# Optimization experiments

Hardware: AMD Instinct MI355X
Metric: run time of the kernel (lower is better)

Reference implementation:

```python
import jax, jax.numpy as jnp
import numpy as np

EMBED_DIM = 1024
HEADS = 16
D_HEAD = EMBED_DIM // HEADS
B, S = 2, 2048


def setup_inputs() -> dict:
    key = jax.random.key(0)
    ks = jax.random.split(key, 7)
    scale = 1.0 / np.sqrt(EMBED_DIM)
    inp = {
        "key": jax.random.normal(ks[0], (B, S, EMBED_DIM), dtype=jnp.float32),
        "query": jax.random.normal(ks[1], (B, S, EMBED_DIM), dtype=jnp.float32),
        "value": jax.random.normal(ks[2], (B, S, EMBED_DIM), dtype=jnp.float32),
        # causal mask, broadcastable to [B, H, Sq, Sk]
        "mask": jnp.tril(jnp.ones((S, S), dtype=bool))[None, None, :, :],
        # torch nn.Linear weights: [out_features, in_features], applied as x @ W.T
        "Wq": jax.random.normal(ks[3], (EMBED_DIM, EMBED_DIM), dtype=jnp.float32) * scale,
        "Wk": jax.random.normal(ks[4], (EMBED_DIM, EMBED_DIM), dtype=jnp.float32) * scale,
        "Wv": jax.random.normal(ks[5], (EMBED_DIM, EMBED_DIM), dtype=jnp.float32) * scale,
        "Wo": jax.random.normal(ks[6], (EMBED_DIM, EMBED_DIM), dtype=jnp.float32) * scale,
    }
    return inp


def reference(key, query, value, mask, Wq, Wk, Wv, Wo):
    b, sq, _ = query.shape
    sk = key.shape[1]
    # projections (torch Linear: x @ W.T), reshape to [B, H, S, Dh]
    q = (query @ Wq.T).reshape(b, sq, HEADS, D_HEAD).transpose(0, 2, 1, 3)
    k = (key @ Wk.T).reshape(b, sk, HEADS, D_HEAD).transpose(0, 2, 1, 3)
    v = (value @ Wv.T).reshape(b, sk, HEADS, D_HEAD).transpose(0, 2, 1, 3)
    # scaled dot-product scores [B, H, Sq, Sk]
    scores = jnp.einsum("bhqd,bhkd->bhqk", q, k) / jnp.sqrt(jnp.float32(D_HEAD))
    scores = jnp.where(mask, scores, jnp.float32(-1e9))
    attn = jax.nn.softmax(scores, axis=-1)
    # dropout p=0.0 -> identity
    out = jnp.einsum("bhqk,bhkd->bhqd", attn, v)  # [B, H, Sq, Dh]
    out = out.transpose(0, 2, 1, 3).reshape(b, sq, EMBED_DIM)
    return out @ Wo.T
```

## Files before the change

kernel.cpp:

```cpp
#include <hip/hip_runtime.h>
#include <stdint.h>


typedef unsigned short ushort_t;
typedef __attribute__((ext_vector_type(8))) __bf16 bf16x8;
typedef __attribute__((ext_vector_type(4))) float floatx4;

#define EMBED 1024
#define SEQ   2048
#define NH    16
#define DH    64
#define QK_SCALE 0.18033688011112042f

__device__ inline ushort_t f2b(float x) {
  unsigned u = __float_as_uint(x);
  u += 0x7FFFu + ((u >> 16) & 1u);
  return (ushort_t)(u >> 16);
}

__device__ inline unsigned pk2(float a, float b) {
  unsigned ua = __float_as_uint(a) + 0x8000u;
  unsigned ub = __float_as_uint(b) + 0x8000u;
  return __builtin_amdgcn_perm(ub, ua, 0x07060302u);
}

__device__ inline void gl_lds16(const ushort_t* g, ushort_t* l) {
  __builtin_amdgcn_global_load_lds(
      (const __attribute__((address_space(1))) unsigned int*)g,
      (__attribute__((address_space(3))) unsigned int*)l, 16, 0, 0);
}

struct CvtArgs {
  const float* src[16];
  ushort_t*    dst[16];
  float        scale[16];
};

__global__ __launch_bounds__(256) void cvt_kernel(CvtArgs a) {
  const int chunk = blockIdx.x >> 9;
  const int off = ((blockIdx.x & 511) << 11) + (threadIdx.x << 3);
  const float sc = a.scale[chunk];
  const float4* s = (const float4*)(a.src[chunk] + off);
  float4 f0 = s[0], f1 = s[1];
  union { ushort_t u[8]; uint4 v; } o;
  o.u[0] = f2b(f0.x * sc); o.u[1] = f2b(f0.y * sc);
  o.u[2] = f2b(f0.z * sc); o.u[3] = f2b(f0.w * sc);
  o.u[4] = f2b(f1.x * sc); o.u[5] = f2b(f1.y * sc);
  o.u[6] = f2b(f1.z * sc); o.u[7] = f2b(f1.w * sc);
  *(uint4*)(a.dst[chunk] + off) = o.v;
}

__device__ inline void store_sub(char* __restrict__ Cv, const int mode,
                                 const int ldc, const int row, const int col,
                                 const floatx4& acc) {
  if (mode == 0) {
    ushort_t* C = (ushort_t*)Cv;
#pragma unroll
    for (int r = 0; r < 4; ++r)
      C[(size_t)(row + r) * ldc + col] = f2b(acc[r]);
  } else if (mode == 1) {
    float* C = (float*)Cv;
#pragma unroll
    for (int r = 0; r < 4; ++r)
      C[(size_t)(row + r) * ldc + col] = acc[r];
  } else {
    ushort_t* C = (ushort_t*)Cv;
    const int b = row >> 11, s = row & 2047;
    const int h = col >> 6, d = col & 63;
    uint2 pk;
    pk.x = pk2(acc[0], acc[1]);
    pk.y = pk2(acc[2], acc[3]);
    *(uint2*)&C[(size_t)((b * NH + h) * DH + d) * SEQ + s] = pk;
  }
}

__device__ inline void gemm512_core(const ushort_t* __restrict__ A,
                                    const ushort_t* __restrict__ W,
                                    char* __restrict__ Cv, const int mode,
                                    const int ldc, const int m0, const int n0) {
  __shared__ ushort_t As[32 * 512];
  __shared__ ushort_t Bs[16 * 512];
  const int tid  = threadIdx.x;
  const int lane = tid & 63;
  const int wid  = tid >> 6;
  const int lm   = lane & 15;
  const int quad = lane >> 4;
  const int wm   = wid >> 1;
  const int wn   = wid & 1;

  floatx4 zero = {0.f, 0.f, 0.f, 0.f};
  floatx4 acc[4][4];
#pragma unroll
  for (int i = 0; i < 4; ++i)
#pragma unroll
    for (int j = 0; j < 4; ++j) acc[i][j] = zero;

  for (int k0 = 0; k0 < EMBED; k0 += 64) {
    __syncthreads();
#pragma unroll
    for (int u = 0; u < 6; ++u) {
      const int c   = wid * 6 + u;
      const int cb  = c & 31;
      const int sub = cb >> 1;
      const int kc  = (cb & 1) * 32 + quad * 8;
      if (c < 32)
        gl_lds16(A + (size_t)(m0 + sub * 16 + lm) * EMBED + k0 + kc, &As[cb * 512]);
      else
        gl_lds16(W + (size_t)(n0 + sub * 16 + lm) * EMBED + k0 + kc, &Bs[cb * 512]);
    }
    __syncthreads();

#pragma unroll
    for (int ks = 0; ks < 2; ++ks) {
      bf16x8 a[4], b[4];
#pragma unroll
      for (int i = 0; i < 4; ++i)
        a[i] = *(const bf16x8*)&As[((wm * 4 + i) * 2 + ks) * 512 + lane * 8];
#pragma unroll
      for (int j = 0; j < 4; ++j)
        b[j] = *(const bf16x8*)&Bs[((wn * 4 + j) * 2 + ks) * 512 + lane * 8];
#pragma unroll
      for (int i = 0; i < 4; ++i)
#pragma unroll
        for (int j = 0; j < 4; ++j)
          acc[i][j] = __builtin_amdgcn_mfma_f32_16x16x32_bf16(a[i], b[j], acc[i][j], 0, 0, 0);
    }
  }

#pragma unroll
  for (int i = 0; i < 4; ++i) {
    const int row = m0 + wm * 64 + i * 16 + quad * 4;
#pragma unroll
    for (int j = 0; j < 4; ++j)
      store_sub(Cv, mode, ldc, row, n0 + wn * 64 + j * 16 + lm, acc[i][j]);
  }
}

struct QkvArgs {
  const ushort_t* A[3];
  const ushort_t* W[3];
  char*           C[3];
};

__global__ __launch_bounds__(512, 4) void qkv_gemm(QkvArgs q) {
  const int z = blockIdx.z;
  gemm512_core(q.A[z], q.W[z], q.C[z], z == 2 ? 2 : 0, EMBED,
               blockIdx.x * 256, blockIdx.y * 128);
}

__global__ __launch_bounds__(256, 4) void o_gemm(const ushort_t* __restrict__ A,
                                                 const ushort_t* __restrict__ W,
                                                 float* __restrict__ C) {
  __shared__ ushort_t As[16 * 512];
  __shared__ ushort_t Bs[8 * 512];
  const int m0 = blockIdx.x * 128, n0 = blockIdx.y * 64;
  const int tid  = threadIdx.x;
  const int lane = tid & 63;
  const int wid  = tid >> 6;
  const int lm   = lane & 15;
  const int quad = lane >> 4;
  const int wm   = wid >> 1;
  const int wn   = wid & 1;

  floatx4 zero = {0.f, 0.f, 0.f, 0.f};
  floatx4 acc[4][2];
#pragma unroll
  for (int i = 0; i < 4; ++i)
#pragma unroll
    for (int j = 0; j < 2; ++j) acc[i][j] = zero;

  for (int k0 = 0; k0 < EMBED; k0 += 64) {
    __syncthreads();
#pragma unroll
    for (int u = 0; u < 6; ++u) {
      const int c   = wid * 6 + u;
      const int cb  = (c < 16) ? c : (c - 16);
      const int sub = cb >> 1;
      const int kc  = (cb & 1) * 32 + quad * 8;
      if (c < 16)
        gl_lds16(A + (size_t)(m0 + sub * 16 + lm) * EMBED + k0 + kc, &As[cb * 512]);
      else
        gl_lds16(W + (size_t)(n0 + sub * 16 + lm) * EMBED + k0 + kc, &Bs[cb * 512]);
    }
    __syncthreads();

#pragma unroll
    for (int ks = 0; ks < 2; ++ks) {
      bf16x8 a[4], b[2];
#pragma unroll
      for (int i = 0; i < 4; ++i)
        a[i] = *(const bf16x8*)&As[((wm * 4 + i) * 2 + ks) * 512 + lane * 8];
#pragma unroll
      for (int j = 0; j < 2; ++j)
        b[j] = *(const bf16x8*)&Bs[((wn * 2 + j) * 2 + ks) * 512 + lane * 8];
#pragma unroll
      for (int i = 0; i < 4; ++i)
#pragma unroll
        for (int j = 0; j < 2; ++j)
          acc[i][j] = __builtin_amdgcn_mfma_f32_16x16x32_bf16(a[i], b[j], acc[i][j], 0, 0, 0);
    }
  }

#pragma unroll
  for (int i = 0; i < 4; ++i) {
    const int row = m0 + wm * 64 + i * 16 + quad * 4;
#pragma unroll
    for (int j = 0; j < 2; ++j) {
      const int col = n0 + wn * 32 + j * 16 + lm;
#pragma unroll
      for (int r = 0; r < 4; ++r)
        C[(size_t)(row + r) * EMBED + col] = acc[i][j][r];
    }
  }
}

__global__ __launch_bounds__(256, 4) void attn_kernel(const ushort_t* __restrict__ Qp,
                                                      const ushort_t* __restrict__ Kp,
                                                      const ushort_t* __restrict__ VpT,
                                                      ushort_t* __restrict__ Ob) {
  __shared__ ushort_t Qs[8 * 512];
  __shared__ ushort_t Ks[2][8 * 512];
  __shared__ ushort_t VTs[2][8 * 512];
  const int L = blockIdx.x;
  const int s8 = (L >> 5) & 7;
  const int g  = L >> 8;
  const int qb = (g == 0) ? s8
               : (g == 1) ? (15 - s8)
               : (g == 2) ? (16 + s8)
                          : (31 - s8);
  const int bh = L & 31;
  const int h = bh & (NH - 1), b = bh >> 4;
  const int tid = threadIdx.x, lane = tid & 63, wid = tid >> 6;
  const int lm = lane & 15, quad = lane >> 4;
  const size_t qkbase = ((size_t)b * SEQ) * EMBED + h * DH;
  const size_t vtbase = ((size_t)(b * NH + h)) * DH * SEQ;

#pragma unroll
  for (int u = 0; u < 2; ++u) {
    const int c = wid * 2 + u;
    gl_lds16(Qp + qkbase + (size_t)(qb * 64 + (c >> 1) * 16 + lm) * EMBED
                 + (c & 1) * 32 + quad * 8,
             &Qs[c * 512]);
  }
#pragma unroll
  for (int u = 0; u < 4; ++u) {
    const int t = wid * 4 + u;
    const int cb = t & 7, sub = cb >> 1, half = cb & 1;
    if (t < 8)
      gl_lds16(Kp + qkbase + (size_t)(sub * 16 + lm) * EMBED + half * 32 + quad * 8,
               &Ks[0][cb * 512]);
    else
      gl_lds16(VpT + vtbase + (size_t)(sub * 16 + lm) * SEQ + half * 32 + quad * 8,
               &VTs[0][cb * 512]);
  }
  asm volatile("s_waitcnt vmcnt(4)" ::: "memory");
  bf16x8 qf[2];
#pragma unroll
  for (int ks = 0; ks < 2; ++ks)
    qf[ks] = *(const bf16x8*)&Qs[(wid * 2 + ks) * 512 + lane * 8];
  ushort_t* pwb = &Qs[wid * 1024];

  float l_part = 0.f;
  floatx4 zero = {0.f, 0.f, 0.f, 0.f};
  floatx4 o_acc[4];
#pragma unroll
  for (int d = 0; d < 4; ++d) o_acc[d] = zero;

  for (int kt = 0; kt <= qb; ++kt) {
    const int cur = kt & 1;
    asm volatile("s_waitcnt vmcnt(0)" ::: "memory");
    __syncthreads();
    if (kt < qb) {
      const int kn = kt + 1;
#pragma unroll
      for (int u = 0; u < 4; ++u) {
        const int t = wid * 4 + u;
        const int cb = t & 7, sub = cb >> 1, half = cb & 1;
        if (t < 8)
          gl_lds16(Kp + qkbase + (size_t)(kn * 64 + sub * 16 + lm) * EMBED
                       + half * 32 + quad * 8,
                   &Ks[cur ^ 1][cb * 512]);
        else
          gl_lds16(VpT + vtbase + (size_t)(sub * 16 + lm) * SEQ
                       + kn * 64 + half * 32 + quad * 8,
                   &VTs[cur ^ 1][cb * 512]);
      }
    }

    floatx4 s_acc[4];
#pragma unroll
    for (int i = 0; i < 4; ++i) s_acc[i] = zero;
#pragma unroll
    for (int ks = 0; ks < 2; ++ks)
#pragma unroll
      for (int i = 0; i < 4; ++i) {
        bf16x8 kf = *(const bf16x8*)&Ks[cur][(i * 2 + ks) * 512 + lane * 8];
        s_acc[i] = __builtin_amdgcn_mfma_f32_16x16x32_bf16(kf, qf[ks], s_acc[i], 0, 0, 0);
      }

    const bool diag = (kt == qb);
#pragma unroll
    for (int i = 0; i < 4; ++i) {
      const int sH = i >> 1;
      const int quadB = ((i & 1) << 1) | (quad >> 1);
      const int gkk = kt * 64 + i * 16 + quad * 4;
      float p[4];
#pragma unroll
      for (int r = 0; r < 4; ++r) p[r] = __builtin_amdgcn_exp2f(s_acc[i][r]);
      if (diag) {
        const int gq = qb * 64 + wid * 16 + lm;
#pragma unroll
        for (int r = 0; r < 4; ++r)
          if (gkk + r > gq) p[r] = 0.f;
      }
#pragma unroll
      for (int r = 0; r < 4; ++r) l_part += p[r];
      uint2 pk;
      pk.x = pk2(p[0], p[1]);
      pk.y = pk2(p[2], p[3]);
      *(uint2*)&pwb[sH * 512 + (quadB * 16 + lm) * 8 + ((quad & 1) << 2)] = pk;
    }
    asm volatile("s_waitcnt lgkmcnt(0)" ::: "memory");

#pragma unroll
    for (int sH = 0; sH < 2; ++sH) {
      bf16x8 pf = *(const bf16x8*)&pwb[sH * 512 + lane * 8];
#pragma unroll
      for (int d = 0; d < 4; ++d) {
        bf16x8 vf = *(const bf16x8*)&VTs[cur][(d * 2 + sH) * 512 + lane * 8];
        o_acc[d] = __builtin_amdgcn_mfma_f32_16x16x32_bf16(vf, pf, o_acc[d], 0, 0, 0);
      }
    }
  }

  {
    float l = l_part;
    l += __shfl_xor(l, 16, 64);
    l += __shfl_xor(l, 32, 64);
    const float inv_l = 1.0f / l;
    const size_t orow = qkbase + (size_t)(qb * 64 + wid * 16 + lm) * EMBED;
#pragma unroll
    for (int d = 0; d < 4; ++d) {
      uint2 pk;
      pk.x = pk2(o_acc[d][0] * inv_l, o_acc[d][1] * inv_l);
      pk.y = pk2(o_acc[d][2] * inv_l, o_acc[d][3] * inv_l);
      *(uint2*)&Ob[orow + d * 16 + quad * 4] = pk;
    }
  }
}

extern "C" void kernel_launch(void* const* d_in, const int* in_sizes, int n_in,
                              void* d_out, int out_size, void* d_ws, size_t ws_size,
                              hipStream_t stream) {
  const float* key   = (const float*)d_in[0];
  const float* query = (const float*)d_in[1];
  const float* value = (const float*)d_in[2];
  const float* Wq = (const float*)d_in[4];
  const float* Wk = (const float*)d_in[5];
  const float* Wv = (const float*)d_in[6];
  const float* Wo = (const float*)d_in[7];

  char* ws = (char*)d_ws;
  const size_t MB = 1024 * 1024;
  ushort_t* Xk  = (ushort_t*)(ws + 0 * MB);
  ushort_t* Xq  = (ushort_t*)(ws + 8 * MB);
  ushort_t* Xv  = (ushort_t*)(ws + 16 * MB);
  ushort_t* Wqb = (ushort_t*)(ws + 24 * MB);
  ushort_t* Wkb = (ushort_t*)(ws + 26 * MB);
  ushort_t* Wvb = (ushort_t*)(ws + 28 * MB);
  ushort_t* Wob = (ushort_t*)(ws + 30 * MB);
  ushort_t* Qp  = (ushort_t*)(ws + 32 * MB);
  ushort_t* Kp  = (ushort_t*)(ws + 40 * MB);
  ushort_t* VpT = (ushort_t*)(ws + 48 * MB);
  ushort_t* Ob  = (ushort_t*)(ws + 56 * MB);

  CvtArgs ca;
  const size_t CE = 1048576;
  for (int c = 0; c < 16; ++c) ca.scale[c] = 1.0f;
  for (int c = 0; c < 4; ++c) { ca.src[c]     = key   + c * CE; ca.dst[c]     = Xk + c * CE; }
  for (int c = 0; c < 4; ++c) { ca.src[4 + c] = query + c * CE; ca.dst[4 + c] = Xq + c * CE; }
  for (int c = 0; c < 4; ++c) { ca.src[8 + c] = value + c * CE; ca.dst[8 + c] = Xv + c * CE; }
  ca.src[12] = Wq; ca.dst[12] = Wqb; ca.scale[12] = QK_SCALE;
  ca.src[13] = Wk; ca.dst[13] = Wkb;
  ca.src[14] = Wv; ca.dst[14] = Wvb;
  ca.src[15] = Wo; ca.dst[15] = Wob;
  cvt_kernel<<<8192, 256, 0, stream>>>(ca);

  QkvArgs qa;
  qa.A[0] = Xq; qa.W[0] = Wqb; qa.C[0] = (char*)Qp;
  qa.A[1] = Xk; qa.W[1] = Wkb; qa.C[1] = (char*)Kp;
  qa.A[2] = Xv; qa.W[2] = Wvb; qa.C[2] = (char*)VpT;
  qkv_gemm<<<dim3(16, 8, 3), 512, 0, stream>>>(qa);

  attn_kernel<<<1024, 256, 0, stream>>>(Qp, Kp, VpT, Ob);

  o_gemm<<<dim3(32, 16), 256, 0, stream>>>(Ob, Wob, (float*)d_out);
}
```

Baseline: 238.8 us.

## Fuse conversion with QKV GEMM and attention with output GEMM via grid barriers

Merges the four kernel launches into two persistent-style kernels. The first does the fp32-to-bf16 conversion and then the QKV projection behind a software grid barrier. The second runs attention, with some blocks handling two tiles, and then the output projection behind a second barrier. This removes launch gaps and tail idle time between stages. In exchange it relies on every block being co-resident, since the spin barrier deadlocks otherwise, and it adds a memset plus atomic spinning.

```diff
diff --git a/kernel.cpp b/kernel.cpp
--- a/kernel.cpp
+++ b/kernel.cpp
@@ -30,24 +30,17 @@
       (__attribute__((address_space(3))) unsigned int*)l, 16, 0, 0);
 }
 
-struct CvtArgs {
-  const float* src[16];
-  ushort_t*    dst[16];
-  float        scale[16];
-};
-
-__global__ __launch_bounds__(256) void cvt_kernel(CvtArgs a) {
-  const int chunk = blockIdx.x >> 9;
-  const int off = ((blockIdx.x & 511) << 11) + (threadIdx.x << 3);
-  const float sc = a.scale[chunk];
-  const float4* s = (const float4*)(a.src[chunk] + off);
-  float4 f0 = s[0], f1 = s[1];
-  union { ushort_t u[8]; uint4 v; } o;
-  o.u[0] = f2b(f0.x * sc); o.u[1] = f2b(f0.y * sc);
-  o.u[2] = f2b(f0.z * sc); o.u[3] = f2b(f0.w * sc);
-  o.u[4] = f2b(f1.x * sc); o.u[5] = f2b(f1.y * sc);
-  o.u[6] = f2b(f1.z * sc); o.u[7] = f2b(f1.w * sc);
-  *(uint4*)(a.dst[chunk] + off) = o.v;
+__device__ inline void grid_arrive_wait(unsigned* cnt, unsigned target) {
+  __syncthreads();
+  __threadfence();
+  if (threadIdx.x == 0) {
+    __hip_atomic_fetch_add(cnt, 1u, __ATOMIC_ACQ_REL, __HIP_MEMORY_SCOPE_AGENT);
+    while (__hip_atomic_load(cnt, __ATOMIC_ACQUIRE, __HIP_MEMORY_SCOPE_AGENT)
+           < target)
+      __builtin_amdgcn_s_sleep(2);
+  }
+  __syncthreads();
+  __threadfence();
 }
 
 __device__ inline void store_sub(char* __restrict__ Cv, const int mode,
@@ -136,92 +129,49 @@
   }
 }
 
-struct QkvArgs {
+struct FusedA {
+  const float*    src[16];
+  ushort_t*       dst[16];
+  float           scale[16];
   const ushort_t* A[3];
   const ushort_t* W[3];
   char*           C[3];
+  unsigned*       bar;
 };
 
-__global__ __launch_bounds__(512, 4) void qkv_gemm(QkvArgs q) {
-  const int z = blockIdx.z;
-  gemm512_core(q.A[z], q.W[z], q.C[z], z == 2 ? 2 : 0, EMBED,
-               blockIdx.x * 256, blockIdx.y * 128);
-}
-
-__global__ __launch_bounds__(256, 4) void o_gemm(const ushort_t* __restrict__ A,
-                                                 const ushort_t* __restrict__ W,
-                                                 float* __restrict__ C) {
-  __shared__ ushort_t As[16 * 512];
-  __shared__ ushort_t Bs[8 * 512];
-  const int m0 = blockIdx.x * 128, n0 = blockIdx.y * 64;
-  const int tid  = threadIdx.x;
-  const int lane = tid & 63;
-  const int wid  = tid >> 6;
-  const int lm   = lane & 15;
-  const int quad = lane >> 4;
-  const int wm   = wid >> 1;
-  const int wn   = wid & 1;
-
-  floatx4 zero = {0.f, 0.f, 0.f, 0.f};
-  floatx4 acc[4][2];
-#pragma unroll
-  for (int i = 0; i < 4; ++i)
-#pragma unroll
-    for (int j = 0; j < 2; ++j) acc[i][j] = zero;
-
-  for (int k0 = 0; k0 < EMBED; k0 += 64) {
-    __syncthreads();
-#pragma unroll
-    for (int u = 0; u < 6; ++u) {
-      const int c   = wid * 6 + u;
-      const int cb  = (c < 16) ? c : (c - 16);
-      const int sub = cb >> 1;
-      const int kc  = (cb & 1) * 32 + quad * 8;
-      if (c < 16)
-        gl_lds16(A + (size_t)(m0 + sub * 16 + lm) * EMBED + k0 + kc, &As[cb * 512]);
-      else
-        gl_lds16(W + (size_t)(n0 + sub * 16 + lm) * EMBED + k0 + kc, &Bs[cb * 512]);
-    }
-    __syncthreads();
-
-#pragma unroll
-    for (int ks = 0; ks < 2; ++ks) {
-      bf16x8 a[4], b[2];
-#pragma unroll
-      for (int i = 0; i < 4; ++i)
-        a[i] = *(const bf16x8*)&As[((wm * 4 + i) * 2 + ks) * 512 + lane * 8];
-#pragma unroll
-      for (int j = 0; j < 2; ++j)
-        b[j] = *(const bf16x8*)&Bs[((wn * 2 + j) * 2 + ks) * 512 + lane * 8];
-#pragma unroll
-      for (int i = 0; i < 4; ++i)
-#pragma unroll
-        for (int j = 0; j < 2; ++j)
-          acc[i][j] = __builtin_amdgcn_mfma_f32_16x16x32_bf16(a[i], b[j], acc[i][j], 0, 0, 0);
-    }
-  }
-
-#pragma unroll
-  for (int i = 0; i < 4; ++i) {
-    const int row = m0 + wm * 64 + i * 16 + quad * 4;
-#pragma unroll
-    for (int j = 0; j < 2; ++j) {
-      const int col = n0 + wn * 32 + j * 16 + lm;
-#pragma unroll
-      for (int r = 0; r < 4; ++r)
-        C[(size_t)(row + r) * EMBED + col] = acc[i][j][r];
-    }
-  }
-}
-
-__global__ __launch_bounds__(256, 4) void attn_kernel(const ushort_t* __restrict__ Qp,
-                                                      const ushort_t* __restrict__ Kp,
-                                                      const ushort_t* __restrict__ VpT,
-                                                      ushort_t* __restrict__ Ob) {
-  __shared__ ushort_t Qs[8 * 512];
-  __shared__ ushort_t Ks[2][8 * 512];
-  __shared__ ushort_t VTs[2][8 * 512];
-  const int L = blockIdx.x;
+__global__ __launch_bounds__(512, 4) void cvt_qkv_kernel(FusedA fa) {
+  {
+    const unsigned idx0 = blockIdx.x * 512u + threadIdx.x;
+#pragma unroll 1
+    for (int p = 0; p < 11; ++p) {
+      const unsigned idx = p * 196608u + idx0;
+      if (idx < 2097152u) {
+        const int chunk = idx >> 17;
+        const unsigned off = (idx & 131071u) << 3;
+        const float sc = fa.scale[chunk];
+        const float4* s = (const float4*)(fa.src[chunk] + off);
+        float4 f0 = s[0], f1 = s[1];
+        union { ushort_t u[8]; uint4 v; } o;
+        o.u[0] = f2b(f0.x * sc); o.u[1] = f2b(f0.y * sc);
+        o.u[2] = f2b(f0.z * sc); o.u[3] = f2b(f0.w * sc);
+        o.u[4] = f2b(f1.x * sc); o.u[5] = f2b(f1.y * sc);
+        o.u[6] = f2b(f1.z * sc); o.u[7] = f2b(f1.w * sc);
+        *(uint4*)(fa.dst[chunk] + off) = o.v;
+      }
+    }
+  }
+  grid_arrive_wait(fa.bar, 384u);
+  const int t = blockIdx.x;
+  const int z = t >> 7, y = (t >> 4) & 7, x = t & 15;
+  gemm512_core(fa.A[z], fa.W[z], fa.C[z], z == 2 ? 2 : 0, EMBED,
+               x * 256, y * 128);
+}
+
+__device__ void attn_body(const ushort_t* __restrict__ Qp,
+                          const ushort_t* __restrict__ Kp,
+                          const ushort_t* __restrict__ VpT,
+                          ushort_t* __restrict__ Ob,
+                          ushort_t* smem, const int L) {
   const int s8 = (L >> 5) & 7;
   const int g  = L >> 8;
   const int qb = (g == 0) ? s8
@@ -234,6 +184,7 @@
   const int lm = lane & 15, quad = lane >> 4;
   const size_t qkbase = ((size_t)b * SEQ) * EMBED + h * DH;
   const size_t vtbase = ((size_t)(b * NH + h)) * DH * SEQ;
+  ushort_t* Qs = smem;
 
 #pragma unroll
   for (int u = 0; u < 2; ++u) {
@@ -244,14 +195,14 @@
   }
 #pragma unroll
   for (int u = 0; u < 4; ++u) {
-    const int t = wid * 4 + u;
-    const int cb = t & 7, sub = cb >> 1, half = cb & 1;
-    if (t < 8)
+    const int tt = wid * 4 + u;
+    const int cb = tt & 7, sub = cb >> 1, half = cb & 1;
+    if (tt < 8)
       gl_lds16(Kp + qkbase + (size_t)(sub * 16 + lm) * EMBED + half * 32 + quad * 8,
-               &Ks[0][cb * 512]);
+               &smem[4096 + cb * 512]);
     else
       gl_lds16(VpT + vtbase + (size_t)(sub * 16 + lm) * SEQ + half * 32 + quad * 8,
-               &VTs[0][cb * 512]);
+               &smem[12288 + cb * 512]);
   }
   asm volatile("s_waitcnt vmcnt(4)" ::: "memory");
   bf16x8 qf[2];
@@ -268,22 +219,26 @@
 
   for (int kt = 0; kt <= qb; ++kt) {
     const int cur = kt & 1;
+    ushort_t* Kc = smem + 4096 + cur * 4096;
+    ushort_t* Vc = smem + 12288 + cur * 4096;
     asm volatile("s_waitcnt vmcnt(0)" ::: "memory");
     __syncthreads();
     if (kt < qb) {
       const int kn = kt + 1;
+      ushort_t* Knx = smem + 4096 + (cur ^ 1) * 4096;
+      ushort_t* Vnx = smem + 12288 + (cur ^ 1) * 4096;
 #pragma unroll
       for (int u = 0; u < 4; ++u) {
-        const int t = wid * 4 + u;
-        const int cb = t & 7, sub = cb >> 1, half = cb & 1;
-        if (t < 8)
+        const int tt = wid * 4 + u;
+        const int cb = tt & 7, sub = cb >> 1, half = cb & 1;
+        if (tt < 8)
           gl_lds16(Kp + qkbase + (size_t)(kn * 64 + sub * 16 + lm) * EMBED
                        + half * 32 + quad * 8,
-                   &Ks[cur ^ 1][cb * 512]);
+                   &Knx[cb * 512]);
         else
           gl_lds16(VpT + vtbase + (size_t)(sub * 16 + lm) * SEQ
                        + kn * 64 + half * 32 + quad * 8,
-                   &VTs[cur ^ 1][cb * 512]);
+                   &Vnx[cb * 512]);
       }
     }
 
@@ -294,7 +249,7 @@
     for (int ks = 0; ks < 2; ++ks)
 #pragma unroll
       for (int i = 0; i < 4; ++i) {
-        bf16x8 kf = *(const bf16x8*)&Ks[cur][(i * 2 + ks) * 512 + lane * 8];
+        bf16x8 kf = *(const bf16x8*)&Kc[(i * 2 + ks) * 512 + lane * 8];
         s_acc[i] = __builtin_amdgcn_mfma_f32_16x16x32_bf16(kf, qf[ks], s_acc[i], 0, 0, 0);
       }
 
@@ -327,7 +282,7 @@
       bf16x8 pf = *(const bf16x8*)&pwb[sH * 512 + lane * 8];
 #pragma unroll
       for (int d = 0; d < 4; ++d) {
-        bf16x8 vf = *(const bf16x8*)&VTs[cur][(d * 2 + sH) * 512 + lane * 8];
+        bf16x8 vf = *(const bf16x8*)&Vc[(d * 2 + sH) * 512 + lane * 8];
         o_acc[d] = __builtin_amdgcn_mfma_f32_16x16x32_bf16(vf, pf, o_acc[d], 0, 0, 0);
       }
     }
@@ -347,6 +302,98 @@
       *(uint2*)&Ob[orow + d * 16 + quad * 4] = pk;
     }
   }
+}
+
+__device__ void o_core(const ushort_t* __restrict__ A,
+                       const ushort_t* __restrict__ W,
+                       float* __restrict__ C, ushort_t* smem,
+                       const int bx, const int by) {
+  ushort_t* As = smem;
+  ushort_t* Bs = smem + 8192;
+  const int m0 = bx * 128, n0 = by * 64;
+  const int tid  = threadIdx.x;
+  const int lane = tid & 63;
+  const int wid  = tid >> 6;
+  const int lm   = lane & 15;
+  const int quad = lane >> 4;
+  const int wm   = wid >> 1;
+  const int wn   = wid & 1;
+
+  floatx4 zero = {0.f, 0.f, 0.f, 0.f};
+  floatx4 acc[4][2];
+#pragma unroll
+  for (int i = 0; i < 4; ++i)
+#pragma unroll
+    for (int j = 0; j < 2; ++j) acc[i][j] = zero;
+
+  for (int k0 = 0; k0 < EMBED; k0 += 64) {
+    __syncthreads();
+#pragma unroll
+    for (int u = 0; u < 6; ++u) {
+      const int c   = wid * 6 + u;
+      const int cb  = (c < 16) ? c : (c - 16);
+      const int sub = cb >> 1;
+      const int kc  = (cb & 1) * 32 + quad * 8;
+      if (c < 16)
+        gl_lds16(A + (size_t)(m0 + sub * 16 + lm) * EMBED + k0 + kc, &As[cb * 512]);
+      else
+        gl_lds16(W + (size_t)(n0 + sub * 16 + lm) * EMBED + k0 + kc, &Bs[cb * 512]);
+    }
+    __syncthreads();
+
+#pragma unroll
+    for (int ks = 0; ks < 2; ++ks) {
+      bf16x8 a[4], b[2];
+#pragma unroll
+      for (int i = 0; i < 4; ++i)
+        a[i] = *(const bf16x8*)&As[((wm * 4 + i) * 2 + ks) * 512 + lane * 8];
+#pragma unroll
+      for (int j = 0; j < 2; ++j)
+        b[j] = *(const bf16x8*)&Bs[((wn * 2 + j) * 2 + ks) * 512 + lane * 8];
+#pragma unroll
+      for (int i = 0; i < 4; ++i)
+#pragma unroll
+        for (int j = 0; j < 2; ++j)
+          acc[i][j] = __builtin_amdgcn_mfma_f32_16x16x32_bf16(a[i], b[j], acc[i][j], 0, 0, 0);
+    }
+  }
+
+#pragma unroll
+  for (int i = 0; i < 4; ++i) {
+    const int row = m0 + wm * 64 + i * 16 + quad * 4;
+#pragma unroll
+    for (int j = 0; j < 2; ++j) {
+      const int col = n0 + wn * 32 + j * 16 + lm;
+#pragma unroll
+      for (int r = 0; r < 4; ++r)
+        C[(size_t)(row + r) * EMBED + col] = acc[i][j][r];
+    }
+  }
+}
+
+struct FusedB {
+  const ushort_t* Qp;
+  const ushort_t* Kp;
+  const ushort_t* VpT;
+  ushort_t*       Ob;
+  const ushort_t* Wob;
+  float*          out;
+  unsigned*       bar;
+};
+
+__global__ __launch_bounds__(256, 4) void attn_o_kernel(FusedB fb) {
+  __shared__ ushort_t smem[20480];
+  const int r = blockIdx.x;
+  if (r < 256) {
+    attn_body(fb.Qp, fb.Kp, fb.VpT, fb.Ob, smem, r);
+    __syncthreads();
+    attn_body(fb.Qp, fb.Kp, fb.VpT, fb.Ob, smem, 256 + r);
+  } else {
+    attn_body(fb.Qp, fb.Kp, fb.VpT, fb.Ob, smem, 256 + r);
+  }
+  grid_arrive_wait(fb.bar, 768u);
+  if (r < 512)
+    o_core(fb.Ob, fb.Wob, fb.out, smem, r & 31, r >> 5);
 }
 
 extern "C" void kernel_launch(void* const* d_in, const int* in_sizes, int n_in,
@@ -373,26 +420,31 @@
   ushort_t* Kp  = (ushort_t*)(ws + 40 * MB);
   ushort_t* VpT = (ushort_t*)(ws + 48 * MB);
   ushort_t* Ob  = (ushort_t*)(ws + 56 * MB);
-
-  CvtArgs ca;
+  unsigned* bar = (unsigned*)(ws + 64 * MB);
+
+  hipMemsetAsync(bar, 0, 128, stream);
+
+  FusedA fa;
   const size_t CE = 1048576;
-  for (int c = 0; c < 16; ++c) ca.scale[c] = 1.0f;
-  for (int c = 0; c < 4; ++c) { ca.src[c]     = key   + c * CE; ca.dst[c]     = Xk + c * CE; }
-  for (int c = 0; c < 4; ++c) { ca.src[4 + c] = query + c * CE; ca.dst[4 + c] = Xq + c * CE; }
-  for (int c = 0; c < 4; ++c) { ca.src[8 + c] = value + c * CE; ca.dst[8 + c] = Xv + c * CE; }
-  ca.src[12] = Wq; ca.dst[12] = Wqb; ca.scale[12] = QK_SCALE;
-  ca.src[13] = Wk; ca.dst[13] = Wkb;
-  ca.src[14] = Wv; ca.dst[14] = Wvb;
-  ca.src[15] = Wo; ca.dst[15] = Wob;
-  cvt_kernel<<<8192, 256, 0, stream>>>(ca);
-
-  QkvArgs qa;
-  qa.A[0] = Xq; qa.W[0] = Wqb; qa.C[0] = (char*)Qp;
-  qa.A[1] = Xk; qa.W[1] = Wkb; qa.C[1] = (char*)Kp;
-  qa.A[2] = Xv; qa.W[2] = Wvb; qa.C[2] = (char*)VpT;
-  qkv_gemm<<<dim3(16, 8, 3), 512, 0, stream>>>(qa);
-
-  attn_kernel<<<1024, 256, 0, stream>>>(Qp, Kp, VpT, Ob);
-
-  o_gemm<<<dim3(32, 16), 256, 0, stream>>>(Ob, Wob, (float*)d_out);
-}
+  for (int c = 0; c < 16; ++c) fa.scale[c] = 1.0f;
+  for (int c = 0; c < 4; ++c) { fa.src[c]     = key   + c * CE; fa.dst[c]     = Xk + c * CE; }
+  for (int c = 0; c < 4; ++c) { fa.src[4 + c] = query + c * CE; fa.dst[4 + c] = Xq + c * CE; }
+  for (int c = 0; c < 4; ++c) { fa.src[8 + c] = value + c * CE; fa.dst[8 + c] = Xv + c * CE; }
+  fa.src[12] = Wq; fa.dst[12] = Wqb; fa.scale[12] = QK_SCALE;
+  fa.src[13] = Wk; fa.dst[13] = Wkb;
+  fa.src[14] = Wv; fa.dst[14] = Wvb;
+  fa.src[15] = Wo; fa.dst[15] = Wob;
+  fa.A[0] = Xq; fa.W[0] = Wqb; fa.C[0] = (char*)Qp;
+  fa.A[1] = Xk; fa.W[1] = Wkb; fa.C[1] = (char*)Kp;
+  fa.A[2] = Xv; fa.W[2] = Wvb; fa.C[2] = (char*)VpT;
+  fa.bar = bar;
+
+  cvt_qkv_kernel<<<384, 512, 0, stream>>>(fa);
+
+  FusedB fb;
+  fb.Qp = Qp; fb.Kp = Kp; fb.VpT = VpT; fb.Ob = Ob;
+  fb.Wob = Wob; fb.out = (float*)d_out;
+  fb.bar = bar + 16;
+
+  attn_o_kernel<<<768, 256, 0, stream>>>(fb);
+}
```

After: 643.9 us. 170% more time.
